# Kernel optimization log

Hardware: AMD Instinct MI355X
Metric: run time of the kernel (lower is better)

The kernel has to match this reference:

```python
import jax, jax.numpy as jnp
import numpy as np

B, T, X, DC, DW, H = 64, 512, 8, 128, 128, 128
NEG = 1e20  # mask constant from the original '-1e20 trick'


def setup_inputs() -> dict:
    key = jax.random.key(0)
    ks = jax.random.split(key, 8)
    inp = jax.random.normal(ks[0], (B, T, DC), dtype=jnp.float32)
    skip_words = jax.random.normal(ks[1], (B, T, X, DW), dtype=jnp.float32)
    rng = np.random.default_rng(0)
    # skip edge source s at position t indexes history slot s+1, which must be <= t -> s <= t-1
    src = rng.integers(0, T, size=(B, T, X))
    src = np.minimum(src, np.maximum(np.arange(T) - 1, 0)[None, :, None]).astype(np.int32)
    cnt = np.minimum(rng.integers(0, X + 1, size=(B, T)), np.arange(T)[None, :]).astype(np.int32)
    s = 0.1
    return {
        'inp': inp,
        'skip_words': skip_words,
        'seq_len': jnp.full((B,), T, dtype=jnp.int32),
        'skip_sources': jnp.asarray(src),
        'skip_count': jnp.asarray(cnt),
        'w_ih_c': jax.random.normal(ks[2], (DC, 3 * H), dtype=jnp.float32) * s,
        'w_hh_c': jax.random.normal(ks[3], (H, 3 * H), dtype=jnp.float32) * s,
        'bias_c': jnp.zeros((3 * H,), dtype=jnp.float32),
        'a_ih': jax.random.normal(ks[4], (DC, H), dtype=jnp.float32) * s,
        'a_hh': jax.random.normal(ks[5], (H, H), dtype=jnp.float32) * s,
        'a_bias': jnp.zeros((H,), dtype=jnp.float32),
        'w_ih_w': jax.random.normal(ks[6], (DW, 3 * H), dtype=jnp.float32) * s,
        'w_hh_w': jax.random.normal(ks[7], (H, 3 * H), dtype=jnp.float32) * s,
        'bias_w': jnp.zeros((3 * H,), dtype=jnp.float32),
    }


def _forward(inp, skip_words, w_ih_c, w_hh_c, bias_c, a_ih, a_hh, a_bias,
             w_ih_w, w_hh_w, bias_w, skip_sources, skip_count):
    Bv, Tv, Xv, _ = skip_words.shape
    Hh = w_hh_c.shape[0]
    # Precompute all input projections (time-independent) outside the scan.
    wi_c_all = jnp.einsum('btd,dk->btk', inp, w_ih_c) + bias_c          # [B,T,3H]
    a_wi_all = jnp.einsum('btd,dh->bth', inp, a_ih) + a_bias            # [B,T,H]
    wi_w_all = jnp.einsum('btxd,dk->btxk', skip_words, w_ih_w) + bias_w  # [B,T,X,3H]
    iota = jnp.arange(Xv)

    def step(carry, xs):
        h_hist, c_hist = carry  # [B, T+1, H] states; slot t+1 written at step t
        t, wi_c, wi_w, a_wi, src, cnt = xs
        h0 = jnp.take(h_hist, t, axis=1)                                 # [B,H]
        idx = (src + 1)[:, :, None]                                      # skip_before_head=False
        c_x = jnp.take_along_axis(c_hist, idx, axis=1)                   # [B,X,H]
        h_x = jnp.take_along_axis(h_hist, idx, axis=1)                   # [B,X,H]
        # WordLSTMCell: c1 = sig(f)*c_x + sig(i)*tanh(g)
        gw = jnp.einsum('bxh,hk->bxk', h_x, w_hh_w) + wi_w               # [B,X,3H]
        f_w, i_w, g_w = jnp.split(gw, 3, axis=-1)
        c1_skip = jax.nn.sigmoid(f_w) * c_x + jax.nn.sigmoid(i_w) * jnp.tanh(g_w)
        # MultiInputLSTMCell: gated merge over {g} U skip cells
        gc = h0 @ w_hh_c + wi_c                                          # [B,3H]
        i_g, o_g, g_g = jnp.split(gc, 3, axis=-1)
        i_g = jax.nn.sigmoid(i_g)[:, None]                               # [B,1,H]
        o_g = jax.nn.sigmoid(o_g)                                        # [B,H]
        g_g = jnp.tanh(g_g)[:, None]                                     # [B,1,H]
        alpha = jax.nn.sigmoid(a_wi[:, None] + jnp.einsum('bxh,hk->bxk', c1_skip, a_hh))
        mask = (iota[None, :] >= cnt[:, None]).astype(alpha.dtype)[:, :, None] * NEG
        ealpha = jnp.exp(jnp.concatenate([i_g, alpha - mask], axis=1))   # [B,1+X,H]
        alpha_n = ealpha / ealpha.sum(axis=1, keepdims=True)
        merged = jnp.concatenate([g_g, c1_skip], axis=1)                 # [B,1+X,H]
        c1 = (merged * alpha_n).sum(axis=1)                              # [B,H]
        h1 = o_g * jnp.tanh(c1)
        h_hist = jax.lax.dynamic_update_slice(h_hist, h1[:, None], (0, t + 1, 0))
        c_hist = jax.lax.dynamic_update_slice(c_hist, c1[:, None], (0, t + 1, 0))
        return (h_hist, c_hist), (h1, c1)

    init = (jnp.zeros((Bv, Tv + 1, Hh), inp.dtype), jnp.zeros((Bv, Tv + 1, Hh), inp.dtype))
    xs = (jnp.arange(Tv), wi_c_all.swapaxes(0, 1), wi_w_all.swapaxes(0, 1),
          a_wi_all.swapaxes(0, 1), skip_sources.swapaxes(0, 1), skip_count.swapaxes(0, 1))
    _, (hs, cs) = jax.lax.scan(step, init, xs)
    return hs.swapaxes(0, 1), cs.swapaxes(0, 1)  # [B,T,H] each


def reference(inp, skip_words, w_ih_c, w_hh_c, bias_c, a_ih, a_hh, a_bias,
              w_ih_w, w_hh_w, bias_w, seq_len, skip_sources, skip_count):
    # seq_len only determines max_seq_len in the torch code; here T is static = inp.shape[1]
    return _forward(inp, skip_words, w_ih_c, w_hh_c, bias_c, a_ih, a_hh, a_bias,
                    w_ih_w, w_hh_w, bias_w, skip_sources, skip_count)
```

## Files before the change

kernel.cpp:

```cpp
#include <hip/hip_runtime.h>

typedef unsigned short u16;
typedef unsigned int u32;
typedef __attribute__((ext_vector_type(8))) short short8;
typedef __attribute__((ext_vector_type(4))) float f32x4;

constexpr int CB = 64, CT = 512, CX = 8, CH = 128;

__device__ __forceinline__ u16 f2b(float f) {
  u32 u = __float_as_uint(f);
  return (u16)((u + 0x7FFFu + ((u >> 16) & 1u)) >> 16);
}
__device__ __forceinline__ float sigf(float x) {
  return __fdividef(1.0f, 1.0f + __expf(-x));
}
__device__ __forceinline__ float tanhfast(float x) {
  return 1.0f - __fdividef(2.0f, __expf(2.0f * x) + 1.0f);
}
__device__ __forceinline__ f32x4 mfma16(short8 a, short8 b, f32x4 c) {
  return __builtin_amdgcn_mfma_f32_16x16x32_bf16(a, b, c, 0, 0, 0);
}

__device__ __forceinline__ void barrier_lgkm() {
  asm volatile("s_waitcnt lgkmcnt(0)" ::: "memory");
  __builtin_amdgcn_s_barrier();
  asm volatile("" ::: "memory");
}

__device__ __forceinline__ void barrier_vm8() {
  asm volatile("s_waitcnt vmcnt(8) lgkmcnt(0)" ::: "memory");
  __builtin_amdgcn_s_barrier();
  asm volatile("" ::: "memory");
}


__global__ void prep_kernel(const float* __restrict__ w_ih_c, const float* __restrict__ w_hh_c,
                            const float* __restrict__ a_ih, const float* __restrict__ a_hh,
                            const float* __restrict__ w_ih_w, const float* __restrict__ w_hh_w,
                            u16* __restrict__ WgwT, u16* __restrict__ WahcT, u16* __restrict__ WcaT) {
  int gid = blockIdx.x * blockDim.x + threadIdx.x;
  if (gid < 98304) {
    int n = gid >> 8, k = gid & 255;
    float v = (k < 128) ? w_hh_w[k * 384 + n] : w_ih_w[(k - 128) * 384 + n];
    WgwT[gid] = f2b(v);
  } else if (gid < 163840) {
    int i = gid - 98304; int n = i >> 7, k = i & 127;
    float v = (n < 128) ? a_hh[k * 128 + n] : w_hh_c[k * 384 + (n - 128)];
    WahcT[i] = f2b(v);
  } else if (gid < 229376) {
    int i = gid - 163840; int n = i >> 7, k = i & 127;
    float v = (n < 384) ? w_ih_c[k * 384 + n] : a_ih[k * 128 + (n - 384)];
    WcaT[i] = f2b(v);
  }
}

__global__ void prep_sw_kernel(const float* __restrict__ sw, u16* __restrict__ swb16) {
  size_t i = ((size_t)blockIdx.x * 1024 + threadIdx.x) * 8;
  float4 x0 = *(const float4*)(sw + i);
  float4 x1 = *(const float4*)(sw + i + 4);
  short8 o;
  o[0] = (short)f2b(x0.x); o[1] = (short)f2b(x0.y); o[2] = (short)f2b(x0.z); o[3] = (short)f2b(x0.w);
  o[4] = (short)f2b(x1.x); o[5] = (short)f2b(x1.y); o[6] = (short)f2b(x1.z); o[7] = (short)f2b(x1.w);
  *(short8*)(swb16 + i) = o;
}

__global__ __launch_bounds__(256) void proj_kernel(const float* __restrict__ inp,
    const u16* __restrict__ WcaT, const float* __restrict__ bias_c,
    const float* __restrict__ a_bias, float* __restrict__ wica) {
  const int m0 = blockIdx.x * 64;
  const int wv = threadIdx.x >> 6, ln = threadIdx.x & 63;
  const int l16 = ln & 15, qd = ln >> 4;
  const int arow = m0 + wv * 16 + l16;
  short8 af[4];
#pragma unroll
  for (int kt = 0; kt < 4; ++kt) {
    const float* p = inp + (size_t)arow * 128 + kt * 32 + qd * 8;
    float4 x0 = *(const float4*)p;
    float4 x1 = *(const float4*)(p + 4);
    short8 a;
    a[0] = (short)f2b(x0.x); a[1] = (short)f2b(x0.y); a[2] = (short)f2b(x0.z); a[3] = (short)f2b(x0.w);
    a[4] = (short)f2b(x1.x); a[5] = (short)f2b(x1.y); a[6] = (short)f2b(x1.z); a[7] = (short)f2b(x1.w);
    af[kt] = a;
  }
  for (int nt = 0; nt < 32; ++nt) {
    const int col = nt * 16 + l16;
    f32x4 acc = {0.f, 0.f, 0.f, 0.f};
#pragma unroll
    for (int kt = 0; kt < 4; ++kt) {
      short8 bf = *(const short8*)(WcaT + (size_t)col * 128 + kt * 32 + qd * 8);
      acc = mfma16(af[kt], bf, acc);
    }
    const float bias = (col < 384) ? bias_c[col] : a_bias[col - 384];
#pragma unroll
    for (int r = 0; r < 4; ++r) {
      const int orow = m0 + wv * 16 + qd * 4 + r;
      wica[(size_t)orow * 512 + col] = acc[r] + bias;
    }
  }
}

__global__ __launch_bounds__(512, 2) void scan_kernel(
    const u16* __restrict__ swb16,
    const int* __restrict__ srcp,
    const int* __restrict__ cntp,
    const float* __restrict__ bias_w,
    const u16* __restrict__ WgwT,
    const u16* __restrict__ WahcT,
    const float* __restrict__ wica,
    float* __restrict__ out)
{
  const int b = blockIdx.x;
  const int tid = threadIdx.x;
  const int wv = tid >> 6;
  const int ln = tid & 63;
  const int l16 = ln & 15;
  const int qd = ln >> 4;
  const int h = wv * 16 + l16;

  float* hs = out + (size_t)b * CT * CH;
  float* cs = out + (size_t)(CB + b) * CT * CH;
  const u16* swb = swb16 + (size_t)b * CT * CX * CH;
  const int* srcb = srcp + b * CT * CX;
  const int* cntb = cntp + b * CT;
  const float* wicab = wica + (size_t)b * CT * 512;

  __shared__ __align__(16) u16 Asg[16 * 136];
  __shared__ __align__(16) u16 Psg[16 * 136];
  __shared__ __align__(16) float Csg[8 * 128];
  __shared__ __align__(16) u16 hbuf[2][128];
  __shared__ __align__(16) float cbuf[2][128];
  __shared__ float gca[512];

  for (int i = tid; i < 16 * 136; i += 512) { Asg[i] = 0; Psg[i] = 0; }
  if (tid < 128) {
    hbuf[0][tid] = 0; hbuf[1][tid] = 0;
    cbuf[0][tid] = 0.0f; cbuf[1][tid] = 0.0f;
  }

  short8 wgwf[3][8];
#pragma unroll
  for (int g = 0; g < 3; ++g) {
    const int n = g * 128 + h;
#pragma unroll
    for (int kt = 0; kt < 8; ++kt)
      wgwf[g][kt] = *(const short8*)(WgwT + (size_t)n * 256 + kt * 32 + qd * 8);
  }
  short8 wacf[4][4];
#pragma unroll
  for (int j = 0; j < 4; ++j) {
    const int n = j * 128 + h;
#pragma unroll
    for (int kt = 0; kt < 4; ++kt)
      wacf[j][kt] = *(const short8*)(WahcT + (size_t)n * 128 + kt * 32 + qd * 8);
  }
  const float bw0 = bias_w[h], bw1 = bias_w[128 + h], bw2 = bias_w[256 + h];

  const u16* swfbase = swb + (size_t)(l16 & 7) * CH + qd * 8;
  short8 swf[4];
#pragma unroll
  for (int kt = 0; kt < 4; ++kt)
    swf[kt] = *(const short8*)(swfbase + kt * 32);

  int src_c = srcb[wv];
  int cnt_c = cntb[0];
  int src_n = srcb[CX + wv];
  int cnt_n = cntb[1];
  float2 h2c, c2c;
  h2c = *(const float2*)(hs + (size_t)src_c * CH + 2 * ln);
  c2c = *(const float2*)(cs + (size_t)src_c * CH + 2 * ln);
  float wicac = wicab[tid];
  float2 h2n = {0.f, 0.f}, c2n = {0.f, 0.f};
  float wican = 0.f;
  int src_n2 = 0, cnt_n2 = 0;
  __syncthreads();

  for (int t = 0; t < CT; ++t) {
    const int par = t & 1;
    const int parp = par ^ 1;

    if (src_c == t - 1) {
      *(u32*)&Asg[wv * 136 + 2 * ln] = *(const u32*)&hbuf[parp][2 * ln];
      *(float2*)&Csg[wv * 128 + 2 * ln] = *(const float2*)&cbuf[parp][2 * ln];
    } else if (src_c == t - 2) {
      *(u32*)&Asg[wv * 136 + 2 * ln] = *(const u32*)&hbuf[par][2 * ln];
      *(float2*)&Csg[wv * 128 + 2 * ln] = *(const float2*)&cbuf[par][2 * ln];
    } else {
      *(u32*)&Asg[wv * 136 + 2 * ln] = (u32)f2b(h2c.x) | ((u32)f2b(h2c.y) << 16);
      *(float2*)&Csg[wv * 128 + 2 * ln] = c2c;
    }
    gca[tid] = wicac;
    if (wv == 7)
      *(u32*)&Asg[8 * 136 + 2 * ln] = *(const u32*)&hbuf[parp][2 * ln];
    barrier_lgkm();

    {
      const int tn = (t + 1 < CT) ? (t + 1) : t;
      const int tn2 = (t + 2 < CT) ? (t + 2) : (CT - 1);
      h2n = *(const float2*)(hs + (size_t)src_n * CH + 2 * ln);
      c2n = *(const float2*)(cs + (size_t)src_n * CH + 2 * ln);
      wican = wicab[(size_t)tn * 512 + tid];
      src_n2 = srcb[tn2 * CX + wv];
      cnt_n2 = cntb[tn2];
    }

    f32x4 d0 = {0.f, 0.f, 0.f, 0.f}, d1 = d0, d2 = d0;
    f32x4 e1 = d0, e2 = d0, e3 = d0;
#pragma unroll
    for (int kt = 0; kt < 4; ++kt) {
      short8 a = *(const short8*)&Asg[l16 * 136 + kt * 32 + qd * 8];
      d0 = mfma16(a, wgwf[0][kt], d0);
      d1 = mfma16(a, wgwf[1][kt], d1);
      d2 = mfma16(a, wgwf[2][kt], d2);
      e1 = mfma16(a, wacf[1][kt], e1);
      e2 = mfma16(a, wacf[2][kt], e2);
      e3 = mfma16(a, wacf[3][kt], e3);
    }
    {
      const int tn = (t + 1 < CT) ? (t + 1) : t;
      const u16* swfn = swfbase + (size_t)tn * CX * CH;
#pragma unroll
      for (int kt = 0; kt < 4; ++kt) {
        d0 = mfma16(swf[kt], wgwf[0][4 + kt], d0);
        d1 = mfma16(swf[kt], wgwf[1][4 + kt], d1);
        d2 = mfma16(swf[kt], wgwf[2][4 + kt], d2);
        swf[kt] = *(const short8*)(swfn + kt * 32);
      }
    }
    const float gi_d = __shfl(e1[0], 32 + l16, 64);
    const float go_d = __shfl(e2[0], 32 + l16, 64);
    const float gg_d = __shfl(e3[0], 32 + l16, 64);
    const float awi = gca[384 + h];
    const float i_g = sigf(gi_d + gca[h]);
    const float o_g = sigf(go_d + gca[128 + h]);
    const float g_g = tanhfast(gg_d + gca[256 + h]);

    float c1s[4] = {0.f, 0.f, 0.f, 0.f};
    if (qd < 2) {
#pragma unroll
      for (int r = 0; r < 4; ++r) {
        const int row = qd * 4 + r;
        const float cx = Csg[row * 128 + h];
        const float fg = sigf(d0[r] + bw0);
        const float ig = sigf(d1[r] + bw1);
        const float gg = tanhfast(d2[r] + bw2);
        const float v = fg * cx + ig * gg;
        c1s[r] = v;
        Psg[row * 136 + h] = f2b(v);
      }
    }
    barrier_lgkm();

    f32x4 e0 = {0.f, 0.f, 0.f, 0.f};
#pragma unroll
    for (int kt = 0; kt < 4; ++kt) {
      short8 a = *(const short8*)&Psg[l16 * 136 + kt * 32 + qd * 8];
      e0 = mfma16(a, wacf[0][kt], e0);
    }
    float pe = 0.0f, pec = 0.0f;
#pragma unroll
    for (int r = 0; r < 4; ++r) {
      const int row = qd * 4 + r;
      if (row < cnt_c) {
        const float al = sigf(e0[r] + awi);
        const float e = __expf(al);
        pe += e;
        pec += e * c1s[r];
      }
    }
    pe += __shfl_xor(pe, 16, 64);  pec += __shfl_xor(pec, 16, 64);
    pe += __shfl_xor(pe, 32, 64);  pec += __shfl_xor(pec, 32, 64);
    const float ei = __expf(i_g);
    const float c1 = __fdividef(ei * g_g + pec, ei + pe);
    const float h1 = o_g * tanhfast(c1);

    if (qd == 0) {
      hs[(size_t)t * CH + h] = h1;
      cs[(size_t)t * CH + h] = c1;
      hbuf[par][h] = f2b(h1);
      cbuf[par][h] = c1;
    }
    barrier_vm8();

    h2c = h2n; c2c = c2n; wicac = wican;
    src_c = src_n; cnt_c = cnt_n; src_n = src_n2; cnt_n = cnt_n2;
  }
}

extern "C" void kernel_launch(void* const* d_in, const int* in_sizes, int n_in,
                              void* d_out, int out_size, void* d_ws, size_t ws_size,
                              hipStream_t stream) {
  (void)in_sizes; (void)n_in; (void)out_size; (void)ws_size;
  const float* inp    = (const float*)d_in[0];
  const float* skw    = (const float*)d_in[1];
  const int*   ssrc   = (const int*)d_in[3];
  const int*   scnt   = (const int*)d_in[4];
  const float* w_ih_c = (const float*)d_in[5];
  const float* w_hh_c = (const float*)d_in[6];
  const float* bias_c = (const float*)d_in[7];
  const float* a_ih   = (const float*)d_in[8];
  const float* a_hh   = (const float*)d_in[9];
  const float* a_bias = (const float*)d_in[10];
  const float* w_ih_w = (const float*)d_in[11];
  const float* w_hh_w = (const float*)d_in[12];
  const float* bias_w = (const float*)d_in[13];

  char* ws = (char*)d_ws;
  u16*   WgwT  = (u16*)(ws);
  u16*   WahcT = (u16*)(ws + 196608);
  u16*   WcaT  = (u16*)(ws + 327680);
  float* wica  = (float*)(ws + 458752);
  u16*   swb16 = (u16*)(ws + 458752 + 67108864);
  float* out   = (float*)d_out;

  prep_kernel<<<224, 1024, 0, stream>>>(w_ih_c, w_hh_c, a_ih, a_hh, w_ih_w, w_hh_w,
                                        WgwT, WahcT, WcaT);
  prep_sw_kernel<<<4096, 1024, 0, stream>>>(skw, swb16);
  proj_kernel<<<512, 256, 0, stream>>>(inp, WcaT, bias_c, a_bias, wica);
  scan_kernel<<<64, 512, 0, stream>>>(swb16, ssrc, scnt, bias_w, WgwT, WahcT, wica, out);
}
```

Measured before the change: 1.785 ms.

## Precompute skip-word input projections in a parallel GEMM and gather bf16 history

Adds a wiw_kernel that computes the skip-word input projections for all B*T*X rows up front with MFMA, so the sequential scan only adds the precomputed values. The scan itself (scan_v2) now runs only the hidden-state half of the skip-cell matmul. The history hidden states are stored as bf16 in global memory, and each step loads that history directly from there. Prefetch depth is relaxed to vmcnt(20). The cost is a large fp32 intermediate (about 400MB) with heavy global traffic, and the original path is kept as a fallback when the workspace is too small.

```diff
diff --git a/kernel.cpp b/kernel.cpp
--- a/kernel.cpp
+++ b/kernel.cpp
@@ -29,6 +29,12 @@
 
 __device__ __forceinline__ void barrier_vm8() {
   asm volatile("s_waitcnt vmcnt(8) lgkmcnt(0)" ::: "memory");
+  __builtin_amdgcn_s_barrier();
+  asm volatile("" ::: "memory");
+}
+
+__device__ __forceinline__ void barrier_vm20() {
+  asm volatile("s_waitcnt vmcnt(20) lgkmcnt(0)" ::: "memory");
   __builtin_amdgcn_s_barrier();
   asm volatile("" ::: "memory");
 }
@@ -99,15 +105,229 @@
   }
 }
 
-__global__ __launch_bounds__(512, 2) void scan_kernel(
-    const u16* __restrict__ swb16,
+__global__ __launch_bounds__(256) void wiw_kernel(const float* __restrict__ skw,
+    const u16* __restrict__ WgwT, float* __restrict__ wiw) {
+  const int m0 = blockIdx.x * 64;
+  const int wv = threadIdx.x >> 6, ln = threadIdx.x & 63;
+  const int l16 = ln & 15, qd = ln >> 4;
+  const int arow = m0 + wv * 16 + l16;
+  short8 af[4];
+#pragma unroll
+  for (int kt = 0; kt < 4; ++kt) {
+    const float* p = skw + (size_t)arow * 128 + kt * 32 + qd * 8;
+    float4 x0 = *(const float4*)p;
+    float4 x1 = *(const float4*)(p + 4);
+    short8 a;
+    a[0] = (short)f2b(x0.x); a[1] = (short)f2b(x0.y); a[2] = (short)f2b(x0.z); a[3] = (short)f2b(x0.w);
+    a[4] = (short)f2b(x1.x); a[5] = (short)f2b(x1.y); a[6] = (short)f2b(x1.z); a[7] = (short)f2b(x1.w);
+    af[kt] = a;
+  }
+  for (int nt = 0; nt < 24; ++nt) {
+    const int col = nt * 16 + l16;
+    f32x4 acc = {0.f, 0.f, 0.f, 0.f};
+#pragma unroll
+    for (int kt = 0; kt < 4; ++kt) {
+      short8 bf = *(const short8*)(WgwT + (size_t)col * 256 + 128 + kt * 32 + qd * 8);
+      acc = mfma16(af[kt], bf, acc);
+    }
+#pragma unroll
+    for (int r = 0; r < 4; ++r) {
+      const int orow = m0 + wv * 16 + qd * 4 + r;
+      wiw[(size_t)orow * 384 + col] = acc[r];
+    }
+  }
+}
+
+__global__ __launch_bounds__(512, 2) void scan_v2(
     const int* __restrict__ srcp,
     const int* __restrict__ cntp,
     const float* __restrict__ bias_w,
     const u16* __restrict__ WgwT,
     const u16* __restrict__ WahcT,
     const float* __restrict__ wica,
+    const float* __restrict__ wiw,
+    u16* __restrict__ hsb16,
     float* __restrict__ out)
+{
+  const int b = blockIdx.x;
+  const int tid = threadIdx.x;
+  const int wv = tid >> 6, ln = tid & 63, l16 = ln & 15, qd = ln >> 4;
+  const int h = wv * 16 + l16;
+  const int row = l16 & 7;
+
+  float* hs = out + (size_t)b * CT * CH;
+  float* cs = out + (size_t)(CB + b) * CT * CH;
+  u16* hsb = hsb16 + (size_t)b * CT * CH;
+  const int* srcb = srcp + b * CT * CX;
+  const int* cntb = cntp + b * CT;
+  const float* wicab = wica + (size_t)b * CT * 512;
+  const float* wiwb = wiw + (size_t)b * CT * CX * 384;
+
+  __shared__ __align__(16) u16 Psg[16 * 136];
+  __shared__ __align__(16) u16 hbuf[2][128];
+  __shared__ __align__(16) float cbuf[2][128];
+
+  for (int i = tid; i < 16 * 136; i += 512) Psg[i] = 0;
+  if (tid < 128) {
+    hbuf[0][tid] = 0; hbuf[1][tid] = 0;
+    cbuf[0][tid] = 0.0f; cbuf[1][tid] = 0.0f;
+  }
+
+  short8 wgwf[3][4];
+#pragma unroll
+  for (int g = 0; g < 3; ++g)
+#pragma unroll
+    for (int kt = 0; kt < 4; ++kt)
+      wgwf[g][kt] = *(const short8*)(WgwT + (size_t)(g * 128 + h) * 256 + kt * 32 + qd * 8);
+  short8 wacf[4][4];
+#pragma unroll
+  for (int j = 0; j < 4; ++j)
+#pragma unroll
+    for (int kt = 0; kt < 4; ++kt)
+      wacf[j][kt] = *(const short8*)(WahcT + (size_t)(j * 128 + h) * 128 + kt * 32 + qd * 8);
+  const float bw0 = bias_w[h], bw1 = bias_w[128 + h], bw2 = bias_w[256 + h];
+
+  int sl_c = srcb[row];
+  int sl_n = srcb[CX + row];
+  int cnt_c = cntb[0], cnt_n = cntb[1];
+  short8 af_g[4];
+#pragma unroll
+  for (int kt = 0; kt < 4; ++kt)
+    af_g[kt] = *(const short8*)(hsb + (size_t)sl_c * CH + kt * 32 + qd * 8);
+  float cg[4];
+#pragma unroll
+  for (int r = 0; r < 4; ++r) {
+    int sr = __shfl(sl_c, (qd * 4 + r) & 7, 64);
+    cg[r] = cs[(size_t)sr * CH + h];
+  }
+  float gt0 = wicab[h], gt1 = wicab[128 + h], gt2 = wicab[256 + h], awi = wicab[384 + h];
+  float ww0[4], ww1[4], ww2[4];
+#pragma unroll
+  for (int r = 0; r < 4; ++r) {
+    const float* wp = wiwb + (size_t)((qd * 4 + r) & 7) * 384 + h;
+    ww0[r] = wp[0]; ww1[r] = wp[128]; ww2[r] = wp[256];
+  }
+  int sl_n2 = 0, cnt_n2 = 0;
+  __syncthreads();
+
+  for (int t = 0; t < CT; ++t) {
+    const int par = t & 1;
+    const int parp = par ^ 1;
+
+    const bool f1 = (sl_c == t - 1), f2 = (sl_c == t - 2);
+    short8 af[4];
+#pragma unroll
+    for (int kt = 0; kt < 4; ++kt) {
+      short8 hA = *(const short8*)&hbuf[parp][kt * 32 + qd * 8];
+      short8 hB = *(const short8*)&hbuf[par][kt * 32 + qd * 8];
+      af[kt] = f1 ? hA : (f2 ? hB : af_g[kt]);
+    }
+    const float cbA = cbuf[parp][h], cbB = cbuf[par][h];
+    if (wv == 7)
+      *(u32*)&Psg[8 * 136 + 2 * ln] = *(const u32*)&hbuf[parp][2 * ln];
+
+    f32x4 d0 = {0.f, 0.f, 0.f, 0.f}, d1 = d0, d2 = d0;
+#pragma unroll
+    for (int kt = 0; kt < 4; ++kt) {
+      d0 = mfma16(af[kt], wgwf[0][kt], d0);
+      d1 = mfma16(af[kt], wgwf[1][kt], d1);
+      d2 = mfma16(af[kt], wgwf[2][kt], d2);
+    }
+    int srs[4];
+#pragma unroll
+    for (int r = 0; r < 4; ++r) srs[r] = __shfl(sl_c, (qd * 4 + r) & 7, 64);
+    float c1s[4] = {0.f, 0.f, 0.f, 0.f};
+    if (qd < 2) {
+#pragma unroll
+      for (int r = 0; r < 4; ++r) {
+        const int rr = qd * 4 + r;
+        const int sr = srs[r];
+        const float cx = (sr == t - 1) ? cbA : (sr == t - 2) ? cbB : cg[r];
+        const float fg = sigf(d0[r] + bw0 + ww0[r]);
+        const float ig = sigf(d1[r] + bw1 + ww1[r]);
+        const float gg = tanhfast(d2[r] + bw2 + ww2[r]);
+        const float v = fg * cx + ig * gg;
+        c1s[r] = v;
+        Psg[rr * 136 + h] = f2b(v);
+      }
+    }
+
+    const int tn = (t + 1 < CT) ? t + 1 : t;
+    const int tn2 = (t + 2 < CT) ? t + 2 : CT - 1;
+#pragma unroll
+    for (int kt = 0; kt < 4; ++kt)
+      af_g[kt] = *(const short8*)(hsb + (size_t)sl_n * CH + kt * 32 + qd * 8);
+#pragma unroll
+    for (int r = 0; r < 4; ++r) {
+      int sr = __shfl(sl_n, (qd * 4 + r) & 7, 64);
+      cg[r] = cs[(size_t)sr * CH + h];
+    }
+#pragma unroll
+    for (int r = 0; r < 4; ++r) {
+      const float* wp = wiwb + ((size_t)tn * CX + ((qd * 4 + r) & 7)) * 384 + h;
+      ww0[r] = wp[0]; ww1[r] = wp[128]; ww2[r] = wp[256];
+    }
+    sl_n2 = srcb[tn2 * CX + row];
+    cnt_n2 = cntb[tn2];
+
+    barrier_lgkm();
+
+    f32x4 e0 = {0.f, 0.f, 0.f, 0.f}, e1 = e0, e2 = e0, e3 = e0;
+#pragma unroll
+    for (int kt = 0; kt < 4; ++kt) {
+      short8 a = *(const short8*)&Psg[l16 * 136 + kt * 32 + qd * 8];
+      e0 = mfma16(a, wacf[0][kt], e0);
+      e1 = mfma16(a, wacf[1][kt], e1);
+      e2 = mfma16(a, wacf[2][kt], e2);
+      e3 = mfma16(a, wacf[3][kt], e3);
+    }
+    const float gi_d = __shfl(e1[0], 32 + l16, 64);
+    const float go_d = __shfl(e2[0], 32 + l16, 64);
+    const float gg_d = __shfl(e3[0], 32 + l16, 64);
+    const float i_g = sigf(gi_d + gt0);
+    const float o_g = sigf(go_d + gt1);
+    const float g_g = tanhfast(gg_d + gt2);
+    float pe = 0.0f, pec = 0.0f;
+#pragma unroll
+    for (int r = 0; r < 4; ++r) {
+      const int rr = qd * 4 + r;
+      if (rr < cnt_c) {
+        const float al = sigf(e0[r] + awi);
+        const float e = __expf(al);
+        pe += e;
+        pec += e * c1s[r];
+      }
+    }
+    pe += __shfl_xor(pe, 16, 64);  pec += __shfl_xor(pec, 16, 64);
+    pe += __shfl_xor(pe, 32, 64);  pec += __shfl_xor(pec, 32, 64);
+    const float ei = __expf(i_g);
+    const float c1 = __fdividef(ei * g_g + pec, ei + pe);
+    const float h1 = o_g * tanhfast(c1);
+
+    gt0 = wicab[(size_t)tn * 512 + h];
+    gt1 = wicab[(size_t)tn * 512 + 128 + h];
+    gt2 = wicab[(size_t)tn * 512 + 256 + h];
+    awi = wicab[(size_t)tn * 512 + 384 + h];
+
+    if (qd == 0) {
+      hs[(size_t)t * CH + h] = h1;
+      cs[(size_t)t * CH + h] = c1;
+      const u16 hb = f2b(h1);
+      hsb[(size_t)t * CH + h] = hb;
+      hbuf[par][h] = hb;
+      cbuf[par][h] = c1;
+    }
+    barrier_vm20();
+
+    sl_c = sl_n; sl_n = sl_n2; cnt_c = cnt_n; cnt_n = cnt_n2;
+  }
+}
+
+__global__ __launch_bounds__(512, 2) void scan_kernel(
+    const u16* __restrict__ swb16, const int* __restrict__ srcp,
+    const int* __restrict__ cntp, const float* __restrict__ bias_w,
+    const u16* __restrict__ WgwT, const u16* __restrict__ WahcT,
+    const float* __restrict__ wica, float* __restrict__ out)
 {
   const int b = blockIdx.x;
   const int tid = threadIdx.x;
@@ -289,7 +509,7 @@
 extern "C" void kernel_launch(void* const* d_in, const int* in_sizes, int n_in,
                               void* d_out, int out_size, void* d_ws, size_t ws_size,
                               hipStream_t stream) {
-  (void)in_sizes; (void)n_in; (void)out_size; (void)ws_size;
+  (void)in_sizes; (void)n_in; (void)out_size;
   const float* inp    = (const float*)d_in[0];
   const float* skw    = (const float*)d_in[1];
   const int*   ssrc   = (const int*)d_in[3];
@@ -309,12 +529,23 @@
   u16*   WahcT = (u16*)(ws + 196608);
   u16*   WcaT  = (u16*)(ws + 327680);
   float* wica  = (float*)(ws + 458752);
-  u16*   swb16 = (u16*)(ws + 458752 + 67108864);
   float* out   = (float*)d_out;
 
   prep_kernel<<<224, 1024, 0, stream>>>(w_ih_c, w_hh_c, a_ih, a_hh, w_ih_w, w_hh_w,
                                         WgwT, WahcT, WcaT);
-  prep_sw_kernel<<<4096, 1024, 0, stream>>>(skw, swb16);
   proj_kernel<<<512, 256, 0, stream>>>(inp, WcaT, bias_c, a_bias, wica);
-  scan_kernel<<<64, 512, 0, stream>>>(swb16, ssrc, scnt, bias_w, WgwT, WahcT, wica, out);
-}
+
+  const size_t NEED_V2 = 458752ull + 67108864ull + 402653184ull + 8388608ull;
+  if (ws_size >= NEED_V2) {
+    float* wiw   = (float*)(ws + 67567616);
+    u16*   hsb16 = (u16*)(ws + 470220800);
+    wiw_kernel<<<4096, 256, 0, stream>>>(skw, WgwT, wiw);
+    scan_v2<<<64, 512, 0, stream>>>(ssrc, scnt, bias_w, WgwT, WahcT, wica, wiw,
+                                    hsb16, out);
+  } else {
+    u16* swb16 = (u16*)(ws + 67567616);
+    prep_sw_kernel<<<4096, 1024, 0, stream>>>(skw, swb16);
+    scan_kernel<<<64, 512, 0, stream>>>(swb16, ssrc, scnt, bias_w, WgwT, WahcT,
+                                        wica, out);
+  }
+}
```

New measurement: 1.930 ms. +8.1%, slower.
